# Kernel optimization log

Hardware: AMD Instinct MI355X
Metric: run time of the kernel (lower is better)

Reference implementation:

```python
import jax, jax.numpy as jnp
import numpy as np

NHEADS = 2
STRENGTH = 0.1
ZED = 8  # zone_embed_dim
STATE_DIM = 137
HID = 256
NBLOCKS = 4
BATCH = 131072


def _mha_seq1(q, k, v, in_w, in_b, out_w, out_b):
    """nn.MultiheadAttention (batch_first) with q,k,v of shape [B,1,E]."""
    B, _, E = q.shape
    hd = E // NHEADS
    Wq, Wk, Wv = in_w[:E], in_w[E:2 * E], in_w[2 * E:]
    bq, bk, bv = in_b[:E], in_b[E:2 * E], in_b[2 * E:]

    def heads(x, W, b):
        return (x @ W.T + b).reshape(B, -1, NHEADS, hd).transpose(0, 2, 1, 3)  # [B,H,1,hd]

    qh, kh, vh = heads(q, Wq, bq), heads(k, Wk, bk), heads(v, Wv, bv)
    scale = 1.0 / jnp.sqrt(jnp.asarray(hd, q.dtype))
    s = jnp.einsum('bhqd,bhkd->bhqk', qh, kh) * scale
    a = jax.nn.softmax(s, axis=-1)  # trivially ones for kv_len=1, kept for fidelity
    o = jnp.einsum('bhqk,bhkd->bhqd', a, vh).transpose(0, 2, 1, 3).reshape(B, -1, E)
    return o @ out_w.T + out_b


def setup_inputs() -> dict:
    key = jax.random.key(0)
    ks = jax.random.split(key, 20)
    S, H, N = STATE_DIM, HID, NBLOCKS
    ahd = S - ZED - 1  # 128

    def w(k, shape, fan_in):
        return jax.random.normal(k, shape, jnp.float32) * (1.0 / np.sqrt(fan_in))

    inp = {
        't': jax.random.uniform(ks[0], (1,), jnp.float32) * 24.0,
        'state': jax.random.normal(ks[1], (BATCH, S), jnp.float32),
        'W0': w(ks[2], (H, S + 2), S + 2), 'b0': jnp.zeros((H,), jnp.float32),
        'blkW1': w(ks[3], (N, H, H), H), 'blkb1': jnp.zeros((N, H), jnp.float32),
        'blkW2': w(ks[4], (N, H, H), H), 'blkb2': jnp.zeros((N, H), jnp.float32),
        'Wout': w(ks[5], (S, H), H), 'bout': jnp.zeros((S,), jnp.float32),
        'lm_in_w': w(ks[6], (3 * ZED, ZED), ZED), 'lm_in_b': jnp.zeros((3 * ZED,), jnp.float32),
        'lm_out_w': w(ks[7], (ZED, ZED), ZED), 'lm_out_b': jnp.zeros((ZED,), jnp.float32),
        'ta_in_w': w(ks[8], (3 * ahd, ahd), ahd), 'ta_in_b': jnp.zeros((3 * ahd,), jnp.float32),
        'ta_out_w': w(ks[9], (ahd, ahd), ahd), 'ta_out_b': jnp.zeros((ahd,), jnp.float32),
    }
    return inp


def reference(t, state, W0, b0, blkW1, blkb1, blkW2, blkb2, Wout, bout,
              lm_in_w, lm_in_b, lm_out_w, lm_out_b,
              ta_in_w, ta_in_b, ta_out_w, ta_out_b):
    B, S = state.shape
    ahd = S - ZED - 1
    two_pi_over_24 = 2.0 * jnp.pi / 24.0
    tv = jnp.concatenate([jnp.sin(t * two_pi_over_24), jnp.cos(t * two_pi_over_24)])  # [2]
    t_vec = jnp.broadcast_to(tv, (B, 2))

    # core dynamics MLP: Linear -> ReLU -> residual blocks -> Linear
    x = jnp.concatenate([state, t_vec], axis=-1)
    h = jax.nn.relu(x @ W0.T + b0)
    for i in range(blkW1.shape[0]):
        inner = jnp.tanh(h @ blkW1[i].T + blkb1[i]) @ blkW2[i].T + blkb2[i]
        h = jnp.tanh(h + inner)
    core = h @ Wout.T + bout

    # attention delta
    hs = state[:, :ahd]
    loc = state[:, ahd:ahd + ZED]
    mov = state[:, -1:]

    q_lm = jnp.broadcast_to(mov, (B, ZED))[:, None, :]
    loc_e = loc[:, None, :]
    enh_loc = _mha_seq1(q_lm, loc_e, loc_e, lm_in_w, lm_in_b, lm_out_w, lm_out_b)[:, 0]
    delta_loc = enh_loc - loc

    t_pad = jnp.concatenate([t_vec, jnp.zeros((B, ahd - 2), state.dtype)], axis=-1)[:, None, :]
    h_e = hs[:, None, :]
    enh_h = _mha_seq1(t_pad, h_e, h_e, ta_in_w, ta_in_b, ta_out_w, ta_out_b)[:, 0]
    delta_h = enh_h - hs

    delta = jnp.concatenate([delta_h, delta_loc, jnp.zeros_like(mov)], axis=-1)
    return core + STRENGTH * delta
```

## Files before the change

### kernel.cpp

```cpp
#include <hip/hip_runtime.h>

typedef __attribute__((ext_vector_type(8))) short short8;
typedef __attribute__((ext_vector_type(4))) float float4_;

#define SDIM    137
#define HID     256
#define K0PAD   160
#define KAUG    416
#define MTILE   64
#define NROWT   (MTILE / 16)
#define NTHR    512

#define SCLF 2.8853900817779268f
#define ISCL 0.34657359027997264f

struct __attribute__((aligned(8))) U2 { unsigned x, y; };

__device__ __forceinline__ unsigned short f2bf(float f) {
  union { float f; unsigned int i; } v; v.f = f;
  return (unsigned short)((v.i + 0x8000u) >> 16);
}
__device__ __forceinline__ unsigned pack_bf16(float a, float b) {
  union { float f; unsigned u; } ua, ub; ua.f = a; ub.f = b;
  return __builtin_amdgcn_perm(ub.u + 0x8000u, ua.u + 0x8000u, 0x07060302u);
}
__device__ __forceinline__ unsigned cvt_pk(float a, float b) {
  unsigned r;
  asm("v_cvt_pk_bf16_f32 %0, %1, %2" : "=v"(r) : "v"(a), "v"(b));
  return r;
}
__device__ __forceinline__ float lo_bf(unsigned p) {
  union { unsigned u; float f; } v; v.u = p << 16; return v.f;
}
__device__ __forceinline__ float hi_bf(unsigned p) {
  union { unsigned u; float f; } v; v.u = p & 0xFFFF0000u; return v.f;
}
__device__ __forceinline__ float stanh(float y) {
#if __has_builtin(__builtin_amdgcn_exp2f)
  float e = __builtin_amdgcn_exp2f(y);
#else
  float e = __expf(y * 0.6931471805599453f);
#endif
  float r = __builtin_amdgcn_rcpf(e + 1.f);
  return __builtin_fmaf(-2.f * SCLF, r, SCLF);
}
__device__ __forceinline__ int sidx(int row, int col) {
  return row * 256 + ((((col >> 3) ^ (row & 31)) << 3) | (col & 7));
}
__device__ __forceinline__ short8 ld_x(const unsigned short* __restrict__ X, int row, int c) {
  return *(const short8*)(X + row * 256 + (((c ^ (row & 31)) << 3)));
}

struct NoEpi { __device__ void operator()(int, float4_ (&)[2]) const {} };

template<int KB0, int KN, int LDB, int BOFF, bool INIT, class EPI>
__device__ __forceinline__ void gemm_half(const unsigned short* __restrict__ X,
                                          const unsigned short* __restrict__ W,
                                          float4_ (&a)[NROWT][2],
                                          int rm, int q, int colbase, EPI epi)
{
  short8 wa[KN][2];
  #pragma unroll
  for (int kb = 0; kb < KN; ++kb)
    #pragma unroll
    for (int mt = 0; mt < 2; ++mt)
      wa[kb][mt] = *(const short8*)(W + (size_t)(colbase + mt * 16 + rm) * LDB
                                      + BOFF + (KB0 + kb) * 32 + q * 8);
  #pragma unroll
  for (int nt = 0; nt < NROWT; ++nt) {
    short8 xb[KN];
    #pragma unroll
    for (int kb = 0; kb < KN; ++kb) xb[kb] = ld_x(X, nt * 16 + rm, (KB0 + kb) * 4 + q);
    if constexpr (INIT) {
      a[nt][0] = (float4_){0.f, 0.f, 0.f, 0.f};
      a[nt][1] = (float4_){0.f, 0.f, 0.f, 0.f};
    }
    #pragma unroll
    for (int kb = 0; kb < KN; ++kb) {
      a[nt][0] = __builtin_amdgcn_mfma_f32_16x16x32_bf16(wa[kb][0], xb[kb], a[nt][0], 0, 0, 0);
      a[nt][1] = __builtin_amdgcn_mfma_f32_16x16x32_bf16(wa[kb][1], xb[kb], a[nt][1], 0, 0, 0);
    }
    if (nt > 0) epi(nt - 1, a[nt - 1]);
  }
  epi(NROWT - 1, a[NROWT - 1]);
}

#define PB_TA   256
#define PB_W0   385
#define PB_BLK  641
#define PB_END  1665

__global__ void prep_all(const float* __restrict__ t,
                         const float* __restrict__ W0,  const float* __restrict__ b0,
                         const float* __restrict__ Wout,const float* __restrict__ bout,
                         const float* __restrict__ lm_in_w, const float* __restrict__ lm_in_b,
                         const float* __restrict__ lm_out_w,const float* __restrict__ lm_out_b,
                         const float* __restrict__ ta_in_w, const float* __restrict__ ta_in_b,
                         const float* __restrict__ ta_out_w,const float* __restrict__ ta_out_b,
                         const float* __restrict__ blkW1, const float* __restrict__ blkW2,
                         unsigned short* __restrict__ W0p,  float* __restrict__ b0p,
                         unsigned short* __restrict__ Waug, float* __restrict__ baug,
                         unsigned short* __restrict__ W1b,  unsigned short* __restrict__ W2b)
{
  const int blk = blockIdx.x;
  const int tt  = threadIdx.x;

  if (blk < PB_TA) {
    int n = blk;
    if (tt < KAUG / 4) {
      int k0 = tt * 4;
      bool patch = (k0 >= 256) && ((n < 128 && k0 < 384) ||
                                   (n >= 128 && n < 136 && k0 >= 384 && k0 < 392));
      if (!patch) {
        U2 p;
        if (k0 < 256 && n < SDIM) {
          float4_ v = *(const float4_*)(Wout + (size_t)n * 256 + k0);
          p.x = pack_bf16(v[0] * ISCL, v[1] * ISCL);
          p.y = pack_bf16(v[2] * ISCL, v[3] * ISCL);
        } else { p.x = 0u; p.y = 0u; }
        *(U2*)(Waug + (size_t)n * KAUG + k0) = p;
      }
    }
  } else if (blk < PB_W0) {
    int b = blk - PB_TA;
    if (b < 128) {
      __shared__ float red[128];
      int n = b, s = tt;
      float dot = 0.f;
      #pragma unroll 8
      for (int r = 0; r < 128; ++r)
        dot += ta_out_w[n * 128 + r] * ta_in_w[(256 + r) * 128 + s];
      Waug[(size_t)n * KAUG + 256 + s] = f2bf(0.1f * (dot - (s == n ? 1.f : 0.f)));

      red[tt] = ta_out_w[n * 128 + tt] * ta_in_b[256 + tt];
      __syncthreads();
      if (tt < 64) {
        float p = red[tt] + red[tt + 64];
        for (int off = 32; off; off >>= 1) p += __shfl_down(p, off);
        if (tt == 0) baug[n] = bout[n] + 0.1f * (p + ta_out_b[n]);
      }
    } else {
      if (tt < 64) {
        int a = tt >> 3, c = tt & 7;
        float dot = 0.f;
        #pragma unroll
        for (int r = 0; r < 8; ++r)
          dot += lm_out_w[a * 8 + r] * lm_in_w[(16 + r) * 8 + c];
        Waug[(size_t)(128 + a) * KAUG + 384 + c] = f2bf(0.1f * (dot - (a == c ? 1.f : 0.f)));
      } else if (tt < 72) {
        int a = tt - 64;
        float dot = 0.f;
        #pragma unroll
        for (int r = 0; r < 8; ++r)
          dot += lm_out_w[a * 8 + r] * lm_in_b[16 + r];
        baug[128 + a] = bout[128 + a] + 0.1f * (dot + lm_out_b[a]);
      } else if (tt == 72) {
        baug[136] = bout[136];
        baug[137] = 0.f; baug[138] = 0.f; baug[139] = 0.f;
      }
    }
  } else if (blk < PB_BLK) {
    int n = blk - PB_W0;
    for (int k = tt; k < K0PAD; k += 128)
      W0p[n * K0PAD + k] = (k < SDIM) ? f2bf(W0[n * 139 + k] * SCLF) : (unsigned short)0;
    if (tt == 0) {
      float tv  = t[0];
      float ang = tv * (6.2831853071795864f / 24.0f);
      float sv = __sinf(ang), cv = __cosf(ang);
      b0p[n] = SCLF * (b0[n] + W0[n * 139 + 137] * sv + W0[n * 139 + 138] * cv);
    }
  } else {
    int i = ((blk - PB_BLK) * 128 + tt) * 4;
    const float* s; unsigned short* d;
    if (i < 262144) { s = blkW1 + i;          d = W1b + i; }
    else            { s = blkW2 + i - 262144; d = W2b + i - 262144; }
    float4_ v = *(const float4_*)s;
    U2 p; p.x = pack_bf16(v[0], v[1]); p.y = pack_bf16(v[2], v[3]);
    *(U2*)d = p;
  }
}


__global__ __launch_bounds__(NTHR)
__attribute__((amdgpu_waves_per_eu(4, 4)))
void fused_odefunc(
    const float* __restrict__ state,
    const unsigned short* __restrict__ W0p,
    const float* __restrict__ b0p,
    const unsigned short* __restrict__ blkW1,
    const float* __restrict__ blkb1,
    const unsigned short* __restrict__ blkW2,
    const float* __restrict__ blkb2,
    const unsigned short* __restrict__ Waug,
    const float* __restrict__ baug,
    float* __restrict__ out)
{
  __shared__ __align__(16) unsigned short ARENA[2 * MTILE * 256];
  unsigned short* H = ARENA;
  unsigned short* G = ARENA + MTILE * 256;

  const int tid  = threadIdx.x;
  const int lane = tid & 63;
  const int wave = tid >> 6;
  const int q    = lane >> 4;
  const int rm   = lane & 15;
  const int cb   = wave * 32;
  const int row0 = blockIdx.x * MTILE;

  #pragma unroll 2
  for (int qd = tid; qd < MTILE * (K0PAD / 4); qd += NTHR) {
    int m  = qd / (K0PAD / 4);
    int k0 = (qd - m * (K0PAD / 4)) * 4;
    const float* sp = state + (size_t)(row0 + m) * SDIM + k0;
    float f0 = (k0     < SDIM) ? sp[0] : 0.f;
    float f1 = (k0 + 1 < SDIM) ? sp[1] : 0.f;
    float f2 = (k0 + 2 < SDIM) ? sp[2] : 0.f;
    float f3 = (k0 + 3 < SDIM) ? sp[3] : 0.f;
    U2 p; p.x = cvt_pk(f0, f1); p.y = cvt_pk(f2, f3);
    *(U2*)(&G[sidx(m, k0)]) = p;
  }
  __syncthreads();

  float4_ a[NROWT][2];

  {
    float4_ bias[2];
    #pragma unroll
    for (int mt = 0; mt < 2; ++mt) bias[mt] = *(const float4_*)(b0p + cb + mt * 16 + q * 4);
    gemm_half<0, 3, K0PAD, 0, true >(G, W0p, a, rm, q, cb, NoEpi{});
    gemm_half<3, 2, K0PAD, 0, false>(G, W0p, a, rm, q, cb, [&](int nt, float4_ (&a2)[2]) {
      int row = nt * 16 + rm;
      #pragma unroll
      for (int mt = 0; mt < 2; ++mt) {
        int col0 = cb + mt * 16 + q * 4;
        float v0 = fmaxf(a2[mt][0] + bias[mt][0], 0.f);
        float v1 = fmaxf(a2[mt][1] + bias[mt][1], 0.f);
        float v2 = fmaxf(a2[mt][2] + bias[mt][2], 0.f);
        float v3 = fmaxf(a2[mt][3] + bias[mt][3], 0.f);
        U2 p; p.x = cvt_pk(v0, v1); p.y = cvt_pk(v2, v3);
        *(U2*)(&H[sidx(row, col0)]) = p;
      }
    });
  }
  __syncthreads();

  for (int blk = 0; blk < 4; ++blk) {
    const unsigned short* W1 = blkW1 + (size_t)blk * 65536;
    const float*          b1 = blkb1 + blk * 256;
    const unsigned short* W2 = blkW2 + (size_t)blk * 65536;
    const float*          b2 = blkb2 + blk * 256;

    {
      float4_ bb[2];
      #pragma unroll
      for (int mt = 0; mt < 2; ++mt) {
        float4_ t4 = *(const float4_*)(b1 + cb + mt * 16 + q * 4);
        bb[mt][0] = t4[0] * SCLF; bb[mt][1] = t4[1] * SCLF;
        bb[mt][2] = t4[2] * SCLF; bb[mt][3] = t4[3] * SCLF;
      }
      gemm_half<0, 4, 256, 0, true >(H, W1, a, rm, q, cb, NoEpi{});
      gemm_half<4, 4, 256, 0, false>(H, W1, a, rm, q, cb, [&](int nt, float4_ (&a2)[2]) {
        int row = nt * 16 + rm;
        #pragma unroll
        for (int mt = 0; mt < 2; ++mt) {
          int col0 = cb + mt * 16 + q * 4;
          float g0 = stanh(a2[mt][0] + bb[mt][0]);
          float g1 = stanh(a2[mt][1] + bb[mt][1]);
          float g2 = stanh(a2[mt][2] + bb[mt][2]);
          float g3 = stanh(a2[mt][3] + bb[mt][3]);
          U2 p; p.x = cvt_pk(g0, g1); p.y = cvt_pk(g2, g3);
          *(U2*)(&G[sidx(row, col0)]) = p;
        }
      });
    }
    __syncthreads();

    {
      float4_ bb[2];
      #pragma unroll
      for (int mt = 0; mt < 2; ++mt) {
        float4_ t4 = *(const float4_*)(b2 + cb + mt * 16 + q * 4);
        bb[mt][0] = t4[0] * SCLF; bb[mt][1] = t4[1] * SCLF;
        bb[mt][2] = t4[2] * SCLF; bb[mt][3] = t4[3] * SCLF;
      }
      gemm_half<0, 4, 256, 0, true >(G, W2, a, rm, q, cb, NoEpi{});
      gemm_half<4, 4, 256, 0, false>(G, W2, a, rm, q, cb, [&](int nt, float4_ (&a2)[2]) {
        int row = nt * 16 + rm;
        #pragma unroll
        for (int mt = 0; mt < 2; ++mt) {
          int col0 = cb + mt * 16 + q * 4;
          int idx = sidx(row, col0);
          U2 old = *(const U2*)(&H[idx]);
          float h0 = stanh(lo_bf(old.x) + a2[mt][0] + bb[mt][0]);
          float h1 = stanh(hi_bf(old.x) + a2[mt][1] + bb[mt][1]);
          float h2 = stanh(lo_bf(old.y) + a2[mt][2] + bb[mt][2]);
          float h3 = stanh(hi_bf(old.y) + a2[mt][3] + bb[mt][3]);
          U2 p; p.x = cvt_pk(h0, h1); p.y = cvt_pk(h2, h3);
          *(U2*)(&H[idx]) = p;
        }
      });
    }
    __syncthreads();
  }

  #pragma unroll 2
  for (int qd = tid; qd < MTILE * (K0PAD / 4); qd += NTHR) {
    int m  = qd / (K0PAD / 4);
    int k0 = (qd - m * (K0PAD / 4)) * 4;
    const float* sp = state + (size_t)(row0 + m) * SDIM + k0;
    float f0 = (k0     < SDIM) ? sp[0] : 0.f;
    float f1 = (k0 + 1 < SDIM) ? sp[1] : 0.f;
    float f2 = (k0 + 2 < SDIM) ? sp[2] : 0.f;
    float f3 = (k0 + 3 < SDIM) ? sp[3] : 0.f;
    U2 p; p.x = cvt_pk(f0, f1); p.y = cvt_pk(f2, f3);
    *(U2*)(&G[sidx(m, k0)]) = p;
  }

  if (cb < 160) {
    gemm_half<0, 4, KAUG, 0, true >(H, Waug, a, rm, q, cb, NoEpi{});
    gemm_half<4, 4, KAUG, 0, false>(H, Waug, a, rm, q, cb, NoEpi{});
  }
  __syncthreads();
  if (cb < 160) {
    gemm_half<0, 3, KAUG, 256, false>(G, Waug, a, rm, q, cb, NoEpi{});
    gemm_half<3, 2, KAUG, 256, false>(G, Waug, a, rm, q, cb, [&](int nt, float4_ (&a2)[2]) {
      float* orow = out + (size_t)(row0 + nt * 16 + rm) * SDIM;
      #pragma unroll
      for (int mt = 0; mt < 2; ++mt) {
        int col0 = cb + mt * 16 + q * 4;
        if (col0 < 136) {
          float4_ b = *(const float4_*)(baug + col0);
          orow[col0 + 0] = a2[mt][0] + b[0];
          orow[col0 + 1] = a2[mt][1] + b[1];
          orow[col0 + 2] = a2[mt][2] + b[2];
          orow[col0 + 3] = a2[mt][3] + b[3];
        } else if (col0 == 136) {
          orow[136] = a2[mt][0] + baug[136];
        }
      }
    });
  }
}

extern "C" void kernel_launch(void* const* d_in, const int* in_sizes, int n_in,
                              void* d_out, int out_size, void* d_ws, size_t ws_size,
                              hipStream_t stream) {
  const float* t        = (const float*)d_in[0];
  const float* state    = (const float*)d_in[1];
  const float* W0       = (const float*)d_in[2];
  const float* b0       = (const float*)d_in[3];
  const float* blkW1    = (const float*)d_in[4];
  const float* blkb1    = (const float*)d_in[5];
  const float* blkW2    = (const float*)d_in[6];
  const float* blkb2    = (const float*)d_in[7];
  const float* Wout     = (const float*)d_in[8];
  const float* bout     = (const float*)d_in[9];
  const float* lm_in_w  = (const float*)d_in[10];
  const float* lm_in_b  = (const float*)d_in[11];
  const float* lm_out_w = (const float*)d_in[12];
  const float* lm_out_b = (const float*)d_in[13];
  const float* ta_in_w  = (const float*)d_in[14];
  const float* ta_in_b  = (const float*)d_in[15];
  const float* ta_out_w = (const float*)d_in[16];
  const float* ta_out_b = (const float*)d_in[17];

  char* ws = (char*)d_ws;
  unsigned short* W0p   = (unsigned short*)ws;
  float*          b0p   = (float*)(ws + 81920);
  unsigned short* Waug  = (unsigned short*)(ws + 82944);
  float*          baug  = (float*)(ws + 295936);
  unsigned short* W1b   = (unsigned short*)(ws + 296960);
  unsigned short* W2b   = (unsigned short*)(ws + 821248);

  prep_all<<<PB_END, 128, 0, stream>>>(t, W0, b0, Wout, bout,
                                       lm_in_w, lm_in_b, lm_out_w, lm_out_b,
                                       ta_in_w, ta_in_b, ta_out_w, ta_out_b,
                                       blkW1, blkW2,
                                       W0p, b0p, Waug, baug, W1b, W2b);

  int batch = in_sizes[1] / SDIM;
  fused_odefunc<<<batch / MTILE, NTHR, 0, stream>>>(
      state, W0p, b0p, W1b, blkb1, W2b, blkb2, Waug, baug,
      (float*)d_out);
}
```

Measured before the change: 466.0 us.

## Retile waves to 32x64 output blocks instead of 64x32 column strips

Each of the 8 waves now covers a 2x4 grid of 16x16 tiles (32 rows by 64 output columns) instead of all 64 rows by 32 columns. Per wave this doubles the weight fragments loaded from global memory while halving the activation fragments read from LDS. The aim is to cut LDS read traffic. The cost is more global/L2 weight loads and more VGPRs for the weight fragments. In the final output GEMM only 6 of 8 waves do work instead of 5 of 8, with part of that work on padding columns.

```diff
diff --git a/kernel.cpp b/kernel.cpp
--- a/kernel.cpp
+++ b/kernel.cpp
@@ -8,7 +8,6 @@
 #define K0PAD   160
 #define KAUG    416
 #define MTILE   64
-#define NROWT   (MTILE / 16)
 #define NTHR    512
 
 #define SCLF 2.8853900817779268f
@@ -51,38 +50,39 @@
   return *(const short8*)(X + row * 256 + (((c ^ (row & 31)) << 3)));
 }
 
-struct NoEpi { __device__ void operator()(int, float4_ (&)[2]) const {} };
+struct NoEpi { __device__ void operator()(int, float4_ (&)[4]) const {} };
 
 template<int KB0, int KN, int LDB, int BOFF, bool INIT, class EPI>
 __device__ __forceinline__ void gemm_half(const unsigned short* __restrict__ X,
                                           const unsigned short* __restrict__ W,
-                                          float4_ (&a)[NROWT][2],
-                                          int rm, int q, int colbase, EPI epi)
+                                          float4_ (&a)[2][4],
+                                          int rm, int q, int cbase, int rbase, EPI epi)
 {
-  short8 wa[KN][2];
+  short8 wa[KN][4];
   #pragma unroll
   for (int kb = 0; kb < KN; ++kb)
     #pragma unroll
-    for (int mt = 0; mt < 2; ++mt)
-      wa[kb][mt] = *(const short8*)(W + (size_t)(colbase + mt * 16 + rm) * LDB
+    for (int mt = 0; mt < 4; ++mt)
+      wa[kb][mt] = *(const short8*)(W + (size_t)(cbase + mt * 16 + rm) * LDB
                                       + BOFF + (KB0 + kb) * 32 + q * 8);
   #pragma unroll
-  for (int nt = 0; nt < NROWT; ++nt) {
+  for (int nt = 0; nt < 2; ++nt) {
     short8 xb[KN];
     #pragma unroll
-    for (int kb = 0; kb < KN; ++kb) xb[kb] = ld_x(X, nt * 16 + rm, (KB0 + kb) * 4 + q);
+    for (int kb = 0; kb < KN; ++kb)
+      xb[kb] = ld_x(X, rbase + nt * 16 + rm, (KB0 + kb) * 4 + q);
     if constexpr (INIT) {
-      a[nt][0] = (float4_){0.f, 0.f, 0.f, 0.f};
-      a[nt][1] = (float4_){0.f, 0.f, 0.f, 0.f};
+      #pragma unroll
+      for (int mt = 0; mt < 4; ++mt) a[nt][mt] = (float4_){0.f, 0.f, 0.f, 0.f};
     }
     #pragma unroll
-    for (int kb = 0; kb < KN; ++kb) {
-      a[nt][0] = __builtin_amdgcn_mfma_f32_16x16x32_bf16(wa[kb][0], xb[kb], a[nt][0], 0, 0, 0);
-      a[nt][1] = __builtin_amdgcn_mfma_f32_16x16x32_bf16(wa[kb][1], xb[kb], a[nt][1], 0, 0, 0);
-    }
+    for (int kb = 0; kb < KN; ++kb)
+      #pragma unroll
+      for (int mt = 0; mt < 4; ++mt)
+        a[nt][mt] = __builtin_amdgcn_mfma_f32_16x16x32_bf16(wa[kb][mt], xb[kb], a[nt][mt], 0, 0, 0);
     if (nt > 0) epi(nt - 1, a[nt - 1]);
   }
-  epi(NROWT - 1, a[NROWT - 1]);
+  epi(1, a[1]);
 }
 
 #define PB_TA   256
@@ -204,7 +204,10 @@
   const int wave = tid >> 6;
   const int q    = lane >> 4;
   const int rm   = lane & 15;
-  const int cb   = wave * 32;
+  const int cg   = wave & 3;
+  const int rg   = wave >> 2;
+  const int cbase = cg * 64;
+  const int rbase = rg * 32;
   const int row0 = blockIdx.x * MTILE;
 
   #pragma unroll 2
@@ -221,26 +224,27 @@
   }
   __syncthreads();
 
-  float4_ a[NROWT][2];
+  float4_ a[2][4];
 
   {
-    float4_ bias[2];
+    float4_ bias[4];
     #pragma unroll
-    for (int mt = 0; mt < 2; ++mt) bias[mt] = *(const float4_*)(b0p + cb + mt * 16 + q * 4);
-    gemm_half<0, 3, K0PAD, 0, true >(G, W0p, a, rm, q, cb, NoEpi{});
-    gemm_half<3, 2, K0PAD, 0, false>(G, W0p, a, rm, q, cb, [&](int nt, float4_ (&a2)[2]) {
-      int row = nt * 16 + rm;
-      #pragma unroll
-      for (int mt = 0; mt < 2; ++mt) {
-        int col0 = cb + mt * 16 + q * 4;
-        float v0 = fmaxf(a2[mt][0] + bias[mt][0], 0.f);
-        float v1 = fmaxf(a2[mt][1] + bias[mt][1], 0.f);
-        float v2 = fmaxf(a2[mt][2] + bias[mt][2], 0.f);
-        float v3 = fmaxf(a2[mt][3] + bias[mt][3], 0.f);
-        U2 p; p.x = cvt_pk(v0, v1); p.y = cvt_pk(v2, v3);
-        *(U2*)(&H[sidx(row, col0)]) = p;
-      }
-    });
+    for (int mt = 0; mt < 4; ++mt) bias[mt] = *(const float4_*)(b0p + cbase + mt * 16 + q * 4);
+    gemm_half<0, 3, K0PAD, 0, true >(G, W0p, a, rm, q, cbase, rbase, NoEpi{});
+    gemm_half<3, 2, K0PAD, 0, false>(G, W0p, a, rm, q, cbase, rbase,
+      [&](int nt, float4_ (&a4)[4]) {
+        int row = rbase + nt * 16 + rm;
+        #pragma unroll
+        for (int mt = 0; mt < 4; ++mt) {
+          int col0 = cbase + mt * 16 + q * 4;
+          float v0 = fmaxf(a4[mt][0] + bias[mt][0], 0.f);
+          float v1 = fmaxf(a4[mt][1] + bias[mt][1], 0.f);
+          float v2 = fmaxf(a4[mt][2] + bias[mt][2], 0.f);
+          float v3 = fmaxf(a4[mt][3] + bias[mt][3], 0.f);
+          U2 p; p.x = cvt_pk(v0, v1); p.y = cvt_pk(v2, v3);
+          *(U2*)(&H[sidx(row, col0)]) = p;
+        }
+      });
   }
   __syncthreads();
 
@@ -251,54 +255,56 @@
     const float*          b2 = blkb2 + blk * 256;
 
     {
-      float4_ bb[2];
+      float4_ bb[4];
       #pragma unroll
-      for (int mt = 0; mt < 2; ++mt) {
-        float4_ t4 = *(const float4_*)(b1 + cb + mt * 16 + q * 4);
+      for (int mt = 0; mt < 4; ++mt) {
+        float4_ t4 = *(const float4_*)(b1 + cbase + mt * 16 + q * 4);
         bb[mt][0] = t4[0] * SCLF; bb[mt][1] = t4[1] * SCLF;
         bb[mt][2] = t4[2] * SCLF; bb[mt][3] = t4[3] * SCLF;
       }
-      gemm_half<0, 4, 256, 0, true >(H, W1, a, rm, q, cb, NoEpi{});
-      gemm_half<4, 4, 256, 0, false>(H, W1, a, rm, q, cb, [&](int nt, float4_ (&a2)[2]) {
-        int row = nt * 16 + rm;
-        #pragma unroll
-        for (int mt = 0; mt < 2; ++mt) {
-          int col0 = cb + mt * 16 + q * 4;
-          float g0 = stanh(a2[mt][0] + bb[mt][0]);
-          float g1 = stanh(a2[mt][1] + bb[mt][1]);
-          float g2 = stanh(a2[mt][2] + bb[mt][2]);
-          float g3 = stanh(a2[mt][3] + bb[mt][3]);
-          U2 p; p.x = cvt_pk(g0, g1); p.y = cvt_pk(g2, g3);
-          *(U2*)(&G[sidx(row, col0)]) = p;
-        }
-      });
+      gemm_half<0, 4, 256, 0, true >(H, W1, a, rm, q, cbase, rbase, NoEpi{});
+      gemm_half<4, 4, 256, 0, false>(H, W1, a, rm, q, cbase, rbase,
+        [&](int nt, float4_ (&a4)[4]) {
+          int row = rbase + nt * 16 + rm;
+          #pragma unroll
+          for (int mt = 0; mt < 4; ++mt) {
+            int col0 = cbase + mt * 16 + q * 4;
+            float g0 = stanh(a4[mt][0] + bb[mt][0]);
+            float g1 = stanh(a4[mt][1] + bb[mt][1]);
+            float g2 = stanh(a4[mt][2] + bb[mt][2]);
+            float g3 = stanh(a4[mt][3] + bb[mt][3]);
+            U2 p; p.x = cvt_pk(g0, g1); p.y = cvt_pk(g2, g3);
+            *(U2*)(&G[sidx(row, col0)]) = p;
+          }
+        });
     }
     __syncthreads();
 
     {
-      float4_ bb[2];
+      float4_ bb[4];
       #pragma unroll
-      for (int mt = 0; mt < 2; ++mt) {
-        float4_ t4 = *(const float4_*)(b2 + cb + mt * 16 + q * 4);
+      for (int mt = 0; mt < 4; ++mt) {
+        float4_ t4 = *(const float4_*)(b2 + cbase + mt * 16 + q * 4);
         bb[mt][0] = t4[0] * SCLF; bb[mt][1] = t4[1] * SCLF;
         bb[mt][2] = t4[2] * SCLF; bb[mt][3] = t4[3] * SCLF;
       }
-      gemm_half<0, 4, 256, 0, true >(G, W2, a, rm, q, cb, NoEpi{});
-      gemm_half<4, 4, 256, 0, false>(G, W2, a, rm, q, cb, [&](int nt, float4_ (&a2)[2]) {
-        int row = nt * 16 + rm;
-        #pragma unroll
-        for (int mt = 0; mt < 2; ++mt) {
-          int col0 = cb + mt * 16 + q * 4;
-          int idx = sidx(row, col0);
-          U2 old = *(const U2*)(&H[idx]);
-          float h0 = stanh(lo_bf(old.x) + a2[mt][0] + bb[mt][0]);
-          float h1 = stanh(hi_bf(old.x) + a2[mt][1] + bb[mt][1]);
-          float h2 = stanh(lo_bf(old.y) + a2[mt][2] + bb[mt][2]);
-          float h3 = stanh(hi_bf(old.y) + a2[mt][3] + bb[mt][3]);
-          U2 p; p.x = cvt_pk(h0, h1); p.y = cvt_pk(h2, h3);
-          *(U2*)(&H[idx]) = p;
-        }
-      });
+      gemm_half<0, 4, 256, 0, true >(G, W2, a, rm, q, cbase, rbase, NoEpi{});
+      gemm_half<4, 4, 256, 0, false>(G, W2, a, rm, q, cbase, rbase,
+        [&](int nt, float4_ (&a4)[4]) {
+          int row = rbase + nt * 16 + rm;
+          #pragma unroll
+          for (int mt = 0; mt < 4; ++mt) {
+            int col0 = cbase + mt * 16 + q * 4;
+            int idx = sidx(row, col0);
+            U2 old = *(const U2*)(&H[idx]);
+            float h0 = stanh(lo_bf(old.x) + a4[mt][0] + bb[mt][0]);
+            float h1 = stanh(hi_bf(old.x) + a4[mt][1] + bb[mt][1]);
+            float h2 = stanh(lo_bf(old.y) + a4[mt][2] + bb[mt][2]);
+            float h3 = stanh(hi_bf(old.y) + a4[mt][3] + bb[mt][3]);
+            U2 p; p.x = cvt_pk(h0, h1); p.y = cvt_pk(h2, h3);
+            *(U2*)(&H[idx]) = p;
+          }
+        });
     }
     __syncthreads();
   }
@@ -316,29 +322,30 @@
     *(U2*)(&G[sidx(m, k0)]) = p;
   }
 
-  if (cb < 160) {
-    gemm_half<0, 4, KAUG, 0, true >(H, Waug, a, rm, q, cb, NoEpi{});
-    gemm_half<4, 4, KAUG, 0, false>(H, Waug, a, rm, q, cb, NoEpi{});
+  if (cg < 3) {
+    gemm_half<0, 4, KAUG, 0, true >(H, Waug, a, rm, q, cbase, rbase, NoEpi{});
+    gemm_half<4, 4, KAUG, 0, false>(H, Waug, a, rm, q, cbase, rbase, NoEpi{});
   }
   __syncthreads();
-  if (cb < 160) {
-    gemm_half<0, 3, KAUG, 256, false>(G, Waug, a, rm, q, cb, NoEpi{});
-    gemm_half<3, 2, KAUG, 256, false>(G, Waug, a, rm, q, cb, [&](int nt, float4_ (&a2)[2]) {
-      float* orow = out + (size_t)(row0 + nt * 16 + rm) * SDIM;
-      #pragma unroll
-      for (int mt = 0; mt < 2; ++mt) {
-        int col0 = cb + mt * 16 + q * 4;
-        if (col0 < 136) {
-          float4_ b = *(const float4_*)(baug + col0);
-          orow[col0 + 0] = a2[mt][0] + b[0];
-          orow[col0 + 1] = a2[mt][1] + b[1];
-          orow[col0 + 2] = a2[mt][2] + b[2];
-          orow[col0 + 3] = a2[mt][3] + b[3];
-        } else if (col0 == 136) {
-          orow[136] = a2[mt][0] + baug[136];
+  if (cg < 3) {
+    gemm_half<0, 3, KAUG, 256, false>(G, Waug, a, rm, q, cbase, rbase, NoEpi{});
+    gemm_half<3, 2, KAUG, 256, false>(G, Waug, a, rm, q, cbase, rbase,
+      [&](int nt, float4_ (&a4)[4]) {
+        float* orow = out + (size_t)(row0 + rbase + nt * 16 + rm) * SDIM;
+        #pragma unroll
+        for (int mt = 0; mt < 4; ++mt) {
+          int col0 = cbase + mt * 16 + q * 4;
+          if (col0 < 136) {
+            float4_ b = *(const float4_*)(baug + col0);
+            orow[col0 + 0] = a4[mt][0] + b[0];
+            orow[col0 + 1] = a4[mt][1] + b[1];
+            orow[col0 + 2] = a4[mt][2] + b[2];
+            orow[col0 + 3] = a4[mt][3] + b[3];
+          } else if (col0 == 136) {
+            orow[136] = a4[mt][0] + baug[136];
+          }
         }
-      }
-    });
+      });
   }
 }
 
```

Result: slower. 719.1 us (+54.3%).

## Double row tile to 128 with 16 waves and load each K-slice of weights once

Applied to the files above, without the earlier changes.

The row tile per block grows from 64 to 128 rows with 1024 threads, and the waves form an 8x2 grid over columns and row halves. The split gemm_half calls are merged into one gemm that loads the full K range of weight fragments into registers at once, so each weight slice is read once per tile instead of twice. The waves_per_eu attribute is dropped. This raises register pressure (up to 16 short8 weight fragments per thread) and doubles LDS use per block, which may cut occupancy. In exchange it halves the number of blocks and the redundant global weight traffic.

```diff
diff --git a/kernel.cpp b/kernel.cpp
--- a/kernel.cpp
+++ b/kernel.cpp
@@ -7,9 +7,8 @@
 #define HID     256
 #define K0PAD   160
 #define KAUG    416
-#define MTILE   64
-#define NROWT   (MTILE / 16)
-#define NTHR    512
+#define MTILE   128
+#define NTHR    1024
 
 #define SCLF 2.8853900817779268f
 #define ISCL 0.34657359027997264f
@@ -53,36 +52,37 @@
 
 struct NoEpi { __device__ void operator()(int, float4_ (&)[2]) const {} };
 
-template<int KB0, int KN, int LDB, int BOFF, bool INIT, class EPI>
-__device__ __forceinline__ void gemm_half(const unsigned short* __restrict__ X,
-                                          const unsigned short* __restrict__ W,
-                                          float4_ (&a)[NROWT][2],
-                                          int rm, int q, int colbase, EPI epi)
+template<int NK, int LDB, int BOFF, bool INIT, class EPI>
+__device__ __forceinline__ void gemm(const unsigned short* __restrict__ X,
+                                     const unsigned short* __restrict__ W,
+                                     float4_ (&a)[4][2],
+                                     int rm, int q, int cbase, int rbase, EPI epi)
 {
-  short8 wa[KN][2];
+  short8 wa[NK][2];
   #pragma unroll
-  for (int kb = 0; kb < KN; ++kb)
+  for (int kb = 0; kb < NK; ++kb)
     #pragma unroll
     for (int mt = 0; mt < 2; ++mt)
-      wa[kb][mt] = *(const short8*)(W + (size_t)(colbase + mt * 16 + rm) * LDB
-                                      + BOFF + (KB0 + kb) * 32 + q * 8);
+      wa[kb][mt] = *(const short8*)(W + (size_t)(cbase + mt * 16 + rm) * LDB
+                                      + BOFF + kb * 32 + q * 8);
   #pragma unroll
-  for (int nt = 0; nt < NROWT; ++nt) {
-    short8 xb[KN];
+  for (int nt = 0; nt < 4; ++nt) {
+    short8 xb[NK];
     #pragma unroll
-    for (int kb = 0; kb < KN; ++kb) xb[kb] = ld_x(X, nt * 16 + rm, (KB0 + kb) * 4 + q);
+    for (int kb = 0; kb < NK; ++kb)
+      xb[kb] = ld_x(X, rbase + nt * 16 + rm, kb * 4 + q);
     if constexpr (INIT) {
       a[nt][0] = (float4_){0.f, 0.f, 0.f, 0.f};
       a[nt][1] = (float4_){0.f, 0.f, 0.f, 0.f};
     }
     #pragma unroll
-    for (int kb = 0; kb < KN; ++kb) {
+    for (int kb = 0; kb < NK; ++kb) {
       a[nt][0] = __builtin_amdgcn_mfma_f32_16x16x32_bf16(wa[kb][0], xb[kb], a[nt][0], 0, 0, 0);
       a[nt][1] = __builtin_amdgcn_mfma_f32_16x16x32_bf16(wa[kb][1], xb[kb], a[nt][1], 0, 0, 0);
     }
     if (nt > 0) epi(nt - 1, a[nt - 1]);
   }
-  epi(NROWT - 1, a[NROWT - 1]);
+  epi(3, a[3]);
 }
 
 #define PB_TA   256
@@ -182,7 +182,6 @@
 
 
 __global__ __launch_bounds__(NTHR)
-__attribute__((amdgpu_waves_per_eu(4, 4)))
 void fused_odefunc(
     const float* __restrict__ state,
     const unsigned short* __restrict__ W0p,
@@ -204,7 +203,10 @@
   const int wave = tid >> 6;
   const int q    = lane >> 4;
   const int rm   = lane & 15;
-  const int cb   = wave * 32;
+  const int cg   = wave & 7;
+  const int rg   = wave >> 3;
+  const int cbase = cg * 32;
+  const int rbase = rg * 64;
   const int row0 = blockIdx.x * MTILE;
 
   #pragma unroll 2
@@ -221,26 +223,26 @@
   }
   __syncthreads();
 
-  float4_ a[NROWT][2];
+  float4_ a[4][2];
 
   {
     float4_ bias[2];
     #pragma unroll
-    for (int mt = 0; mt < 2; ++mt) bias[mt] = *(const float4_*)(b0p + cb + mt * 16 + q * 4);
-    gemm_half<0, 3, K0PAD, 0, true >(G, W0p, a, rm, q, cb, NoEpi{});
-    gemm_half<3, 2, K0PAD, 0, false>(G, W0p, a, rm, q, cb, [&](int nt, float4_ (&a2)[2]) {
-      int row = nt * 16 + rm;
-      #pragma unroll
-      for (int mt = 0; mt < 2; ++mt) {
-        int col0 = cb + mt * 16 + q * 4;
-        float v0 = fmaxf(a2[mt][0] + bias[mt][0], 0.f);
-        float v1 = fmaxf(a2[mt][1] + bias[mt][1], 0.f);
-        float v2 = fmaxf(a2[mt][2] + bias[mt][2], 0.f);
-        float v3 = fmaxf(a2[mt][3] + bias[mt][3], 0.f);
-        U2 p; p.x = cvt_pk(v0, v1); p.y = cvt_pk(v2, v3);
-        *(U2*)(&H[sidx(row, col0)]) = p;
-      }
-    });
+    for (int mt = 0; mt < 2; ++mt) bias[mt] = *(const float4_*)(b0p + cbase + mt * 16 + q * 4);
+    gemm<K0PAD / 32, K0PAD, 0, true>(G, W0p, a, rm, q, cbase, rbase,
+      [&](int nt, float4_ (&a2)[2]) {
+        int row = rbase + nt * 16 + rm;
+        #pragma unroll
+        for (int mt = 0; mt < 2; ++mt) {
+          int col0 = cbase + mt * 16 + q * 4;
+          float v0 = fmaxf(a2[mt][0] + bias[mt][0], 0.f);
+          float v1 = fmaxf(a2[mt][1] + bias[mt][1], 0.f);
+          float v2 = fmaxf(a2[mt][2] + bias[mt][2], 0.f);
+          float v3 = fmaxf(a2[mt][3] + bias[mt][3], 0.f);
+          U2 p; p.x = cvt_pk(v0, v1); p.y = cvt_pk(v2, v3);
+          *(U2*)(&H[sidx(row, col0)]) = p;
+        }
+      });
   }
   __syncthreads();
 
@@ -254,24 +256,24 @@
       float4_ bb[2];
       #pragma unroll
       for (int mt = 0; mt < 2; ++mt) {
-        float4_ t4 = *(const float4_*)(b1 + cb + mt * 16 + q * 4);
+        float4_ t4 = *(const float4_*)(b1 + cbase + mt * 16 + q * 4);
         bb[mt][0] = t4[0] * SCLF; bb[mt][1] = t4[1] * SCLF;
         bb[mt][2] = t4[2] * SCLF; bb[mt][3] = t4[3] * SCLF;
       }
-      gemm_half<0, 4, 256, 0, true >(H, W1, a, rm, q, cb, NoEpi{});
-      gemm_half<4, 4, 256, 0, false>(H, W1, a, rm, q, cb, [&](int nt, float4_ (&a2)[2]) {
-        int row = nt * 16 + rm;
-        #pragma unroll
-        for (int mt = 0; mt < 2; ++mt) {
-          int col0 = cb + mt * 16 + q * 4;
-          float g0 = stanh(a2[mt][0] + bb[mt][0]);
-          float g1 = stanh(a2[mt][1] + bb[mt][1]);
-          float g2 = stanh(a2[mt][2] + bb[mt][2]);
-          float g3 = stanh(a2[mt][3] + bb[mt][3]);
-          U2 p; p.x = cvt_pk(g0, g1); p.y = cvt_pk(g2, g3);
-          *(U2*)(&G[sidx(row, col0)]) = p;
-        }
-      });
+      gemm<8, 256, 0, true>(H, W1, a, rm, q, cbase, rbase,
+        [&](int nt, float4_ (&a2)[2]) {
+          int row = rbase + nt * 16 + rm;
+          #pragma unroll
+          for (int mt = 0; mt < 2; ++mt) {
+            int col0 = cbase + mt * 16 + q * 4;
+            float g0 = stanh(a2[mt][0] + bb[mt][0]);
+            float g1 = stanh(a2[mt][1] + bb[mt][1]);
+            float g2 = stanh(a2[mt][2] + bb[mt][2]);
+            float g3 = stanh(a2[mt][3] + bb[mt][3]);
+            U2 p; p.x = cvt_pk(g0, g1); p.y = cvt_pk(g2, g3);
+            *(U2*)(&G[sidx(row, col0)]) = p;
+          }
+        });
     }
     __syncthreads();
 
@@ -279,26 +281,26 @@
       float4_ bb[2];
       #pragma unroll
       for (int mt = 0; mt < 2; ++mt) {
-        float4_ t4 = *(const float4_*)(b2 + cb + mt * 16 + q * 4);
+        float4_ t4 = *(const float4_*)(b2 + cbase + mt * 16 + q * 4);
         bb[mt][0] = t4[0] * SCLF; bb[mt][1] = t4[1] * SCLF;
         bb[mt][2] = t4[2] * SCLF; bb[mt][3] = t4[3] * SCLF;
       }
-      gemm_half<0, 4, 256, 0, true >(G, W2, a, rm, q, cb, NoEpi{});
-      gemm_half<4, 4, 256, 0, false>(G, W2, a, rm, q, cb, [&](int nt, float4_ (&a2)[2]) {
-        int row = nt * 16 + rm;
-        #pragma unroll
-        for (int mt = 0; mt < 2; ++mt) {
-          int col0 = cb + mt * 16 + q * 4;
-          int idx = sidx(row, col0);
-          U2 old = *(const U2*)(&H[idx]);
-          float h0 = stanh(lo_bf(old.x) + a2[mt][0] + bb[mt][0]);
-          float h1 = stanh(hi_bf(old.x) + a2[mt][1] + bb[mt][1]);
-          float h2 = stanh(lo_bf(old.y) + a2[mt][2] + bb[mt][2]);
-          float h3 = stanh(hi_bf(old.y) + a2[mt][3] + bb[mt][3]);
-          U2 p; p.x = cvt_pk(h0, h1); p.y = cvt_pk(h2, h3);
-          *(U2*)(&H[idx]) = p;
-        }
-      });
+      gemm<8, 256, 0, true>(G, W2, a, rm, q, cbase, rbase,
+        [&](int nt, float4_ (&a2)[2]) {
+          int row = rbase + nt * 16 + rm;
+          #pragma unroll
+          for (int mt = 0; mt < 2; ++mt) {
+            int col0 = cbase + mt * 16 + q * 4;
+            int idx = sidx(row, col0);
+            U2 old = *(const U2*)(&H[idx]);
+            float h0 = stanh(lo_bf(old.x) + a2[mt][0] + bb[mt][0]);
+            float h1 = stanh(hi_bf(old.x) + a2[mt][1] + bb[mt][1]);
+            float h2 = stanh(lo_bf(old.y) + a2[mt][2] + bb[mt][2]);
+            float h3 = stanh(hi_bf(old.y) + a2[mt][3] + bb[mt][3]);
+            U2 p; p.x = cvt_pk(h0, h1); p.y = cvt_pk(h2, h3);
+            *(U2*)(&H[idx]) = p;
+          }
+        });
     }
     __syncthreads();
   }
@@ -316,30 +318,27 @@
     *(U2*)(&G[sidx(m, k0)]) = p;
   }
 
-  if (cb < 160) {
-    gemm_half<0, 4, KAUG, 0, true >(H, Waug, a, rm, q, cb, NoEpi{});
-    gemm_half<4, 4, KAUG, 0, false>(H, Waug, a, rm, q, cb, NoEpi{});
-  }
+  if (cg < 5)
+    gemm<8, KAUG, 0, true>(H, Waug, a, rm, q, cbase, rbase, NoEpi{});
   __syncthreads();
-  if (cb < 160) {
-    gemm_half<0, 3, KAUG, 256, false>(G, Waug, a, rm, q, cb, NoEpi{});
-    gemm_half<3, 2, KAUG, 256, false>(G, Waug, a, rm, q, cb, [&](int nt, float4_ (&a2)[2]) {
-      float* orow = out + (size_t)(row0 + nt * 16 + rm) * SDIM;
-      #pragma unroll
-      for (int mt = 0; mt < 2; ++mt) {
-        int col0 = cb + mt * 16 + q * 4;
-        if (col0 < 136) {
-          float4_ b = *(const float4_*)(baug + col0);
-          orow[col0 + 0] = a2[mt][0] + b[0];
-          orow[col0 + 1] = a2[mt][1] + b[1];
-          orow[col0 + 2] = a2[mt][2] + b[2];
-          orow[col0 + 3] = a2[mt][3] + b[3];
-        } else if (col0 == 136) {
-          orow[136] = a2[mt][0] + baug[136];
+  if (cg < 5)
+    gemm<5, KAUG, 256, false>(G, Waug, a, rm, q, cbase, rbase,
+      [&](int nt, float4_ (&a2)[2]) {
+        float* orow = out + (size_t)(row0 + rbase + nt * 16 + rm) * SDIM;
+        #pragma unroll
+        for (int mt = 0; mt < 2; ++mt) {
+          int col0 = cbase + mt * 16 + q * 4;
+          if (col0 < 136) {
+            float4_ b = *(const float4_*)(baug + col0);
+            orow[col0 + 0] = a2[mt][0] + b[0];
+            orow[col0 + 1] = a2[mt][1] + b[1];
+            orow[col0 + 2] = a2[mt][2] + b[2];
+            orow[col0 + 3] = a2[mt][3] + b[3];
+          } else if (col0 == 136) {
+            orow[136] = a2[mt][0] + baug[136];
+          }
         }
-      }
-    });
-  }
+      });
 }
 
 extern "C" void kernel_launch(void* const* d_in, const int* in_sizes, int n_in,
```

Result: slower. 530.4 us (+13.8%).
